# Performance work log

Measured on AMD Instinct MI355X. Metric: run time of the kernel, lower is better.

## Reference

```python
import jax, jax.numpy as jnp
import numpy as np

EPS = 1e-5

def conv1x1(x, W, b):
    # x: [B,C,H,W], W: [O,C], b: [O] -- a 1x1 conv is a per-pixel matmul
    return jnp.einsum('bchw,oc->bohw', x, W) + b[None, :, None, None]

def mean_variance_norm(feat):
    # torch .var(dim=2) is unbiased (ddof=1)
    m = feat.mean(axis=(2, 3), keepdims=True)
    v = feat.var(axis=(2, 3), ddof=1, keepdims=True)
    return (feat - m) / jnp.sqrt(v + EPS)

def setup_inputs() -> dict:
    key = jax.random.key(0)
    ks = jax.random.split(key, 10)
    B, C, H, W = 4, 256, 64, 64
    sc = 1.0 / np.sqrt(C)
    return {
        'content': jax.random.normal(ks[0], (B, C, H, W), jnp.float32),
        'style': jax.random.normal(ks[1], (B, C, H, W), jnp.float32),
        'content_key': jax.random.normal(ks[2], (B, C, H, W), jnp.float32),
        'style_key': jax.random.normal(ks[3], (B, C, H, W), jnp.float32),
        'Wf': jax.random.normal(ks[4], (C, C), jnp.float32) * sc,
        'bf': jnp.zeros((C,), jnp.float32),
        'Wg': jax.random.normal(ks[5], (C, C), jnp.float32) * sc,
        'bg': jnp.zeros((C,), jnp.float32),
        'Wh': jax.random.normal(ks[6], (C, C), jnp.float32) * sc,
        'bh': jnp.zeros((C,), jnp.float32),
    }

def reference(content, style, content_key, style_key, Wf, bf, Wg, bg, Wh, bh):
    Fq = conv1x1(content_key, Wf, bf)   # [B,Ck,H,W]
    G = conv1x1(style_key, Wg, bg)      # [B,Ck,Hs,Ws]
    Hv = conv1x1(style, Wh, bh)         # [B,C,Hs,Ws]
    b, _, h, w = Fq.shape
    _, C, hs, ws = Hv.shape
    N, M = h * w, hs * ws
    q = Fq.reshape(b, -1, N).transpose(0, 2, 1)   # [B,N,Ck]
    k = G.reshape(b, -1, M)                        # [B,Ck,M]
    style_flat = Hv.reshape(b, C, M).transpose(0, 2, 1)  # [B,M,C]
    # masks are all-ones -> attn_mask all zeros -> no masking (faithful to None path)
    S = jax.nn.softmax(jnp.einsum('bnc,bcm->bnm', q, k), axis=-1)  # [B,N,M]
    mean = jnp.einsum('bnm,bmc->bnc', S, style_flat)               # [B,N,C]
    std = jnp.sqrt(jax.nn.relu(
        jnp.einsum('bnm,bmc->bnc', S, style_flat * style_flat) - mean * mean))
    mean = mean.reshape(b, h, w, C).transpose(0, 3, 1, 2)  # [B,C,H,W]
    std = std.reshape(b, h, w, C).transpose(0, 3, 1, 2)
    return std * mean_variance_norm(content) + mean
```

## Files before the change

### kernel.cpp

```cpp
#include <hip/hip_runtime.h>


typedef unsigned int u32;
typedef unsigned short u16;
typedef _Float16 f16x8 __attribute__((ext_vector_type(8)));
typedef float f32x4 __attribute__((ext_vector_type(4)));
typedef float f32x16 __attribute__((ext_vector_type(16)));
typedef unsigned int u32x2 __attribute__((ext_vector_type(2)));
typedef unsigned __attribute__((address_space(3))) as3_u32;
typedef const unsigned __attribute__((address_space(1))) as1_u32;

#define L2E 1.44269504088896340736f
#define MFMA(a, b, c) __builtin_amdgcn_mfma_f32_16x16x32_f16(a, b, c, 0, 0, 0)
#define MFMA32(a, b, c) __builtin_amdgcn_mfma_f32_32x32x16_f16(a, b, c, 0, 0, 0)
#define EXP2(x) __builtin_amdgcn_exp2f(x)

__device__ __forceinline__ u16 h_bits(_Float16 h) { return __builtin_bit_cast(u16, h); }
__device__ __forceinline__ u16 f2h(float f) { return h_bits((_Float16)f); }
__device__ __forceinline__ u32 pk2(float a, float b) {
    return (u32)f2h(a) | ((u32)f2h(b) << 16);
}

__device__ __forceinline__ f16x8 ldh8(const u16* p) {
    uint4 v = *(const uint4*)p;
    return __builtin_bit_cast(f16x8, v);
}

__device__ __forceinline__ void gll16(const u16* g, const void* lds) {
    __builtin_amdgcn_global_load_lds((as1_u32*)g,
                                     (as3_u32*)(unsigned)(unsigned long long)lds,
                                     16, 0, 0);
}

__device__ __forceinline__ u32x2 pl32_swap(u32 a, u32 b) {
#if __has_builtin(__builtin_amdgcn_permlane32_swap)
    return __builtin_amdgcn_permlane32_swap(a, b, false, false);
#else
    asm("v_permlane32_swap_b32 %0, %1" : "+v"(a), "+v"(b));
    u32x2 r; r.x = a; r.y = b; return r;
#endif
}

__global__ void k_prep(const float* __restrict__ content,
                       const float* __restrict__ style, const float* __restrict__ ckey,
                       const float* __restrict__ skey,
                       const float* __restrict__ Wf, const float* __restrict__ Wg,
                       const float* __restrict__ Wh,
                       u16* __restrict__ X1, u16* __restrict__ X2, u16* __restrict__ Cc,
                       u16* __restrict__ Wb,
                       float* __restrict__ cm, float* __restrict__ cr) {
    int z = blockIdx.z, t = threadIdx.x;
    if (z >= 15) {
        int blk = (z - 15) * 256 + blockIdx.y * 64 + blockIdx.x;
        const float* p = content + (size_t)blk * 4096;
        float s = 0.f, ss = 0.f;
        for (int i = 0; i < 4; i++) {
            float4 v = *(const float4*)(p + (i * 256 + t) * 4);
            s  += (v.x + v.y) + (v.z + v.w);
            ss += (v.x * v.x + v.y * v.y) + (v.z * v.z + v.w * v.w);
        }
        for (int d = 32; d >= 1; d >>= 1) { s += __shfl_xor(s, d); ss += __shfl_xor(ss, d); }
        __shared__ __align__(16) float as[4], ass[4];
        int w = t >> 6;
        if ((t & 63) == 0) { as[w] = s; ass[w] = ss; }
        __syncthreads();
        if (t == 0) {
            s  = (as[0] + as[1]) + (as[2] + as[3]);
            ss = (ass[0] + ass[1]) + (ass[2] + ass[3]);
            float mean = s * (1.0f / 4096.0f);
            float var = (ss - s * mean) * (1.0f / 4095.0f);
            cm[blk] = mean;
            cr[blk] = rsqrtf(var + 1e-5f);
        }
        return;
    }
    if (z >= 12) {
        if (blockIdx.y != 0) return;
        int m = z - 12;
        const float* src = (m == 0) ? Wf : ((m == 1) ? Wg : Wh);
        u16* dst = Wb + m * 65536;
        int i = (blockIdx.x * 256 + t) * 4;
        float4 v = *(const float4*)(src + i);
        ushort4 o;
        o.x = f2h(v.x); o.y = f2h(v.y); o.z = f2h(v.z); o.w = f2h(v.w);
        *(ushort4*)(dst + i) = o;
        return;
    }
    int tensor = z >> 2, b = z & 3;
    const float* src = ((tensor == 0) ? style : ((tensor == 1) ? ckey : skey))
                       + (size_t)b * 256 * 4096;
    u16* dst = ((tensor == 0) ? X1 : ((tensor == 1) ? X2 : Cc)) + (size_t)b * 4096 * 256;
    int c0 = blockIdx.y * 64, t0 = blockIdx.x * 64;
    __shared__ __align__(16) float ls[64][65];
    int tr = t >> 4, tc = t & 15;
    for (int i = 0; i < 4; i++) {
        int c_off = i * 16 + tr;
        float4 v = *(const float4*)(src + (size_t)(c0 + c_off) * 4096 + t0 + tc * 4);
        ls[tc * 4 + 0][c_off] = v.x;
        ls[tc * 4 + 1][c_off] = v.y;
        ls[tc * 4 + 2][c_off] = v.z;
        ls[tc * 4 + 3][c_off] = v.w;
    }
    __syncthreads();
    for (int i = 0; i < 4; i++) {
        int tokrow = i * 16 + tr;
        ushort4 o;
        o.x = f2h(ls[tokrow][tc * 4 + 0]);
        o.y = f2h(ls[tokrow][tc * 4 + 1]);
        o.z = f2h(ls[tokrow][tc * 4 + 2]);
        o.w = f2h(ls[tokrow][tc * 4 + 3]);
        *(ushort4*)(dst + (size_t)(t0 + tokrow) * 256 + c0 + tc * 4) = o;
    }
}

__launch_bounds__(256)
__global__ void k_gemm(const u16* X1, const u16* X2, u16* Cc,
                       u16* A, u16* Bv, const u16* __restrict__ Wb,
                       const float* __restrict__ bfp, const float* __restrict__ bgp,
                       const float* __restrict__ bhp) {
    int mode = blockIdx.z, b = blockIdx.y, tok0 = blockIdx.x * 64;
    const u16* X = ((mode == 0) ? X2 : ((mode == 1) ? (const u16*)Cc : X1))
                   + (size_t)b * 4096 * 256;
    const u16* W = Wb + mode * 65536;
    const float* bias = (mode == 0) ? bfp : ((mode == 1) ? bgp : bhp);
    int t = threadIdx.x, w = t >> 6, lane = t & 63, ln = lane & 15, quad = lane >> 4;

    f32x4 acc[4][4];
    for (int i = 0; i < 4; i++)
        for (int j = 0; j < 4; j++) acc[i][j] = f32x4{0.f, 0.f, 0.f, 0.f};

    #pragma unroll
    for (int ks = 0; ks < 8; ks++) {
        f16x8 wf[4];
        #pragma unroll
        for (int ct = 0; ct < 4; ct++)
            wf[ct] = ldh8(W + (size_t)(w * 64 + ct * 16 + ln) * 256 + ks * 32 + quad * 8);
        #pragma unroll
        for (int rt = 0; rt < 4; rt++) {
            f16x8 xf = ldh8(X + (size_t)(tok0 + rt * 16 + ln) * 256 + ks * 32 + quad * 8);
            if (mode < 2) {
                #pragma unroll
                for (int ct = 0; ct < 4; ct++) acc[rt][ct] = MFMA(xf, wf[ct], acc[rt][ct]);
            } else {
                #pragma unroll
                for (int ct = 0; ct < 4; ct++) acc[rt][ct] = MFMA(wf[ct], xf, acc[rt][ct]);
            }
        }
    }

    __syncthreads();

    if (mode < 2) {
        u16* O = ((mode == 0) ? A : Cc) + (size_t)b * 4096 * 256;
        float bv[4];
        #pragma unroll
        for (int ct = 0; ct < 4; ct++) bv[ct] = bias[w * 64 + ct * 16 + ln];
        #pragma unroll
        for (int rt = 0; rt < 4; rt++)
            #pragma unroll
            for (int ct = 0; ct < 4; ct++)
                #pragma unroll
                for (int r = 0; r < 4; r++) {
                    int tok = tok0 + rt * 16 + quad * 4 + r;
                    int o = w * 64 + ct * 16 + ln;
                    O[(size_t)tok * 256 + o] = f2h(acc[rt][ct][r] + bv[ct]);
                }
    } else {
        u16* OV = Bv + (size_t)b * 256 * 4096;
        #pragma unroll
        for (int ct = 0; ct < 4; ct++)
            #pragma unroll
            for (int r = 0; r < 4; r++) {
                int o = w * 64 + ct * 16 + quad * 4 + r;
                float bb = bias[o];
                #pragma unroll
                for (int rt = 0; rt < 4; rt++) {
                    int tok = tok0 + rt * 16 + ln;
                    OV[(size_t)o * 4096 + tok] = f2h(acc[rt][ct][r] + bb);
                }
            }
    }
}

__launch_bounds__(512)
__attribute__((amdgpu_waves_per_eu(2)))
__global__ void k_flash(const u16* __restrict__ Qt, const u16* __restrict__ Kt,
                        const u16* __restrict__ Vt,
                        const float* __restrict__ content, const float* __restrict__ cm,
                        const float* __restrict__ cr, float* __restrict__ out) {
    __shared__ __align__(16) char smem[131072];
    const u16* KsU = (const u16*)smem;
    int t = threadIdx.x, w8 = t >> 6, l = t & 63, lq = l & 31, h = l >> 5;
    int qg = w8 & 3, mh = w8 >> 2;

    int b = blockIdx.y, q0 = blockIdx.x * 128, coff = blockIdx.z * 128;

    const u16* Kg = Kt + (size_t)b * 4096 * 256;
    const u16* Vg = Vt + ((size_t)b * 256 + coff) * 4096;

    const u16* ksrc;
    {
        int qb = w8 * 1024 + l * 16;
        int r0 = qb >> 9;
        int swz = (qb & 511) ^ ((r0 & 7) << 4);
        ksrc = Kg + r0 * 256 + (swz >> 1);
    }
    const char* ldsKw = smem + w8 * 1024;

    int uu = (h ^ (lq & 7)) << 3;
    int tab0 = uu, tab1 = 16 ^ uu, tab2 = 32 ^ uu, tab3 = 48 ^ uu;
    int kb0 = (mh * 64 + lq) * 256;

    f16x8 qf[16];
    {
        const u16* qp = Qt + ((size_t)b * 4096 + q0 + qg * 32 + lq) * 256 + h * 8;
        #pragma unroll
        for (int ks = 0; ks < 16; ks++) qf[ks] = ldh8(qp + ks * 16);
    }

    f32x16 am[4], aq[4];
    #pragma unroll
    for (int i = 0; i < 16; i++) {
        am[0][i] = 0.f; am[1][i] = 0.f; am[2][i] = 0.f; am[3][i] = 0.f;
        aq[0][i] = 0.f; aq[1][i] = 0.f; aq[2][i] = 0.f; aq[3][i] = 0.f;
    }
    float mrow = -1e30f, lrow = 0.f;

    #pragma unroll
    for (int i = 0; i < 8; i++) gll16(ksrc + i * 4096, ldsKw + i * 8192);
    asm volatile("s_waitcnt vmcnt(0)" ::: "memory");
    __builtin_amdgcn_s_barrier();

    int koffB = 0;
    for (int it = 0; it < 32; it++) {
        if (it < 31) {
            int m0n = (it + 1) * 32768;
            #pragma unroll
            for (int i = 0; i < 8; i++)
                gll16(ksrc + m0n + i * 4096, ldsKw + (koffB ^ 65536) + i * 8192);
        }
        asm volatile("" ::: "memory");

        #pragma unroll
        for (int ph = 0; ph < 2; ph++) {
            int kb = (koffB >> 1) + kb0 + ph * 8192;
            f32x16 sA, sB;
            #pragma unroll
            for (int i = 0; i < 16; i++) { sA[i] = 0.f; sB[i] = 0.f; }
            __builtin_amdgcn_s_setprio(1);
            #pragma unroll
            for (int ks = 0; ks < 8; ks++) {
                int off = ((ks & 3) == 0 ? tab0 : (ks & 3) == 1 ? tab1
                          : (ks & 3) == 2 ? tab2 : tab3) + (ks >> 2) * 64;
                sA = MFMA32(ldh8(KsU + kb + off), qf[ks], sA);
            }
            #pragma unroll
            for (int ks = 8; ks < 16; ks++) {
                int off = ((ks & 3) == 0 ? tab0 : (ks & 3) == 1 ? tab1
                          : (ks & 3) == 2 ? tab2 : tab3) + (ks >> 2) * 64;
                sB = MFMA32(ldh8(KsU + kb + off), qf[ks], sB);
            }
            __builtin_amdgcn_s_setprio(0);
            f32x16 s;
            #pragma unroll
            for (int i = 0; i < 16; i++) s[i] = sA[i] + sB[i];

            const u16* Vit = Vg + it * 128 + mh * 64 + ph * 32;
            f16x8 vfr[2][4];
            #pragma unroll
            for (int ks = 0; ks < 2; ks++)
                #pragma unroll
                for (int ct = 0; ct < 4; ct++)
                    vfr[ks][ct] = ldh8(Vit + (size_t)(ct * 32 + lq) * 4096 + ks * 16 + h * 8);

            float m8[8];
            #pragma unroll
            for (int r = 0; r < 8; r++) m8[r] = fmaxf(s[r], s[r + 8]);
            #pragma unroll
            for (int d = 4; d >= 1; d >>= 1)
                #pragma unroll
                for (int r = 0; r < d; r++) m8[r] = fmaxf(m8[r], m8[r + d]);
            float mt = fmaxf(m8[0], __shfl_xor(m8[0], 32));

            float mn, al;
            bool resc = !__all(mt - mrow <= 8.0f);
            if (resc) {
                mn = fmaxf(mrow, mt);
                al = EXP2((mrow - mn) * L2E);
                mrow = mn;
            } else {
                mn = mrow;
                al = 1.0f;
            }
            float base = mn * L2E;
            #pragma unroll
            for (int r = 0; r < 16; r++)
                s[r] = (float)(_Float16)EXP2(__builtin_fmaf(s[r], L2E, -base));
            float a8[8];
            #pragma unroll
            for (int r = 0; r < 8; r++) a8[r] = s[r] + s[r + 8];
            #pragma unroll
            for (int d = 4; d >= 1; d >>= 1)
                #pragma unroll
                for (int r = 0; r < d; r++) a8[r] += a8[r + d];
            float rs = a8[0] + __shfl_xor(a8[0], 32);
            lrow = lrow * al + rs;

            if (resc) {
                #pragma unroll
                for (int r = 0; r < 16; r++) {
                    float sc = __shfl(al, 8 * (r >> 2) + 4 * h + (r & 3));
                    am[0][r] *= sc; am[1][r] *= sc; am[2][r] *= sc; am[3][r] *= sc;
                    aq[0][r] *= sc; aq[1][r] *= sc; aq[2][r] *= sc; aq[3][r] *= sc;
                }
            }

            f16x8 pfr[2];
            {
                u32 d0 = pk2(s[0], s[1]),   d1 = pk2(s[2], s[3]);
                u32 d2 = pk2(s[4], s[5]),   d3 = pk2(s[6], s[7]);
                u32 d4 = pk2(s[8], s[9]),   d5 = pk2(s[10], s[11]);
                u32 d6 = pk2(s[12], s[13]), d7 = pk2(s[14], s[15]);
                u32x2 p02 = pl32_swap(d0, d2);
                u32x2 p13 = pl32_swap(d1, d3);
                u32x2 p46 = pl32_swap(d4, d6);
                u32x2 p57 = pl32_swap(d5, d7);
                uint4 fa = {p02.x, p13.x, p02.y, p13.y};
                uint4 fb = {p46.x, p57.x, p46.y, p57.y};
                pfr[0] = __builtin_bit_cast(f16x8, fa);
                pfr[1] = __builtin_bit_cast(f16x8, fb);
            }

            __builtin_amdgcn_s_setprio(1);
            #pragma unroll
            for (int ks = 0; ks < 2; ks++) {
                f16x8 pf = pfr[ks];
                #pragma unroll
                for (int ct = 0; ct < 4; ct++) {
                    f16x8 vf = vfr[ks][ct];
                    am[ct] = MFMA32(pf, vf, am[ct]);
                    f16x8 vh = vf * vf;
                    f16x8 vl = __builtin_elementwise_fma(vf, vf, -vh);
                    aq[ct] = MFMA32(pf, vh, aq[ct]);
                    aq[ct] = MFMA32(pf, vl, aq[ct]);
                }
            }
            __builtin_amdgcn_s_setprio(0);
        }

        asm volatile("s_waitcnt vmcnt(0)" ::: "memory");
        __builtin_amdgcn_s_barrier();
        koffB ^= 65536;
    }

    float* P1  = (float*)smem;
    float* Lsm = (float*)(smem + 32768);
    float* Ms  = (float*)(smem + 36864);
    float* Ss  = (float*)(smem + 70656);
    __syncthreads();
    if (h == 0) {
        Lsm[w8 * 32 + lq] = lrow;
        Lsm[256 + w8 * 32 + lq] = mrow;
    }
    __syncthreads();
    int pw = w8 ^ 4;
    float lP = Lsm[pw * 32 + lq];
    float mP = Lsm[256 + pw * 32 + lq];
    float M = fmaxf(mrow, mP);
    float scOwn = EXP2((mrow - M) * L2E);
    float lC = lrow * scOwn + lP * EXP2((mP - M) * L2E);
    {
        #pragma unroll
        for (int r = 0; r < 16; r++) {
            float sc = __shfl(scOwn, 8 * (r >> 2) + 4 * h + (r & 3));
            am[0][r] *= sc; am[1][r] *= sc; am[2][r] *= sc; am[3][r] *= sc;
            aq[0][r] *= sc; aq[1][r] *= sc; aq[2][r] *= sc; aq[3][r] *= sc;
        }
    }
    float inv = 1.0f / lC;
    float iv[16];
    #pragma unroll
    for (int r = 0; r < 16; r++) iv[r] = __shfl(inv, (r & 3) + 8 * (r >> 2) + 4 * h);

    #pragma unroll
    for (int g = 0; g < 2; g++) {
        #pragma unroll
        for (int ct = 0; ct < 2; ct++) {
            int a = 2 * g + ct;
            __syncthreads();
            if (mh == 1) {
                #pragma unroll
                for (int rq = 0; rq < 4; rq++) {
                    int o = qg * 1024 + lq * 32 + 8 * rq + 4 * h;
                    f32x4 va = {am[a][4 * rq], am[a][4 * rq + 1],
                                am[a][4 * rq + 2], am[a][4 * rq + 3]};
                    f32x4 vq = {aq[a][4 * rq], aq[a][4 * rq + 1],
                                aq[a][4 * rq + 2], aq[a][4 * rq + 3]};
                    *(f32x4*)(P1 + o) = va;
                    *(f32x4*)(P1 + 4096 + o) = vq;
                }
            }
            __syncthreads();
            if (mh == 0) {
                #pragma unroll
                for (int rq = 0; rq < 4; rq++) {
                    int o = qg * 1024 + lq * 32 + 8 * rq + 4 * h;
                    f32x4 va = *(const f32x4*)(P1 + o);
                    f32x4 vq = *(const f32x4*)(P1 + 4096 + o);
                    #pragma unroll
                    for (int j = 0; j < 4; j++) {
                        am[a][4 * rq + j] += va[j];
                        aq[a][4 * rq + j] += vq[j];
                    }
                }
            }
        }
        __syncthreads();
        if (mh == 0) {
            #pragma unroll
            for (int ct = 0; ct < 2; ct++) {
                int a = 2 * g + ct;
                #pragma unroll
                for (int rq = 0; rq < 4; rq++) {
                    f32x4 mv, sv;
                    #pragma unroll
                    for (int j = 0; j < 4; j++) {
                        int r = 4 * rq + j;
                        float mean = am[a][r] * iv[r];
                        float ex2 = aq[a][r] * iv[r];
                        float var = ex2 - mean * mean;
                        mv[j] = mean;
                        sv[j] = sqrtf(fmaxf(var, 0.f));
                    }
                    int c = ct * 32 + lq;
                    int qloc = qg * 32 + 8 * rq + 4 * h;
                    *(f32x4*)(Ms + c * 132 + qloc) = mv;
                    *(f32x4*)(Ss + c * 132 + qloc) = sv;
                }
            }
        }
        __syncthreads();
        #pragma unroll
        for (int pass = 0; pass < 4; pass++) {
            int c = pass * 16 + (t >> 5);
            int qloc = (t & 31) * 4;
            f32x4 mv = *(const f32x4*)(Ms + c * 132 + qloc);
            f32x4 sv = *(const f32x4*)(Ss + c * 132 + qloc);
            int gc = coff + g * 64 + c;
            size_t basei = ((size_t)b * 256 + gc) * 4096 + q0 + qloc;
            float4 cv = *(const float4*)(content + basei);
            float cmv = cm[b * 256 + gc], crv = cr[b * 256 + gc];
            float4 o;
            o.x = sv[0] * ((cv.x - cmv) * crv) + mv[0];
            o.y = sv[1] * ((cv.y - cmv) * crv) + mv[1];
            o.z = sv[2] * ((cv.z - cmv) * crv) + mv[2];
            o.w = sv[3] * ((cv.w - cmv) * crv) + mv[3];
            *(float4*)(out + basei) = o;
        }
    }
}

extern "C" void kernel_launch(void* const* d_in, const int* in_sizes, int n_in,
                              void* d_out, int out_size, void* d_ws, size_t ws_size,
                              hipStream_t stream) {
    const float* content = (const float*)d_in[0];
    const float* style   = (const float*)d_in[1];
    const float* ckey    = (const float*)d_in[2];
    const float* skey    = (const float*)d_in[3];
    const float* Wf      = (const float*)d_in[4];
    const float* bfp     = (const float*)d_in[5];
    const float* Wg      = (const float*)d_in[6];
    const float* bgp     = (const float*)d_in[7];
    const float* Wh      = (const float*)d_in[8];
    const float* bhp     = (const float*)d_in[9];
    float* out = (float*)d_out;
    char* ws = (char*)d_ws;

    float* cm = (float*)(ws + 0);
    float* cr = (float*)(ws + 4096);
    u16*   Wb = (u16*)(ws + 8192);
    u16*   A  = (u16*)(ws + 1048576);
    u16*   Bv = (u16*)(ws + 9437184);
    u16*   Cc = (u16*)(ws + 17825792);
    u16*   X1 = (u16*)d_out;
    u16*   X2 = (u16*)d_out + 4194304;

    k_prep<<<dim3(64, 4, 19), 256, 0, stream>>>(content, style, ckey, skey,
                                                Wf, Wg, Wh, X1, X2, Cc, Wb, cm, cr);
    k_gemm<<<dim3(64, 4, 3), 256, 0, stream>>>(X1, X2, Cc, A, Bv, Wb, bfp, bgp, bhp);
    k_flash<<<dim3(32, 4, 2), 512, 0, stream>>>(A, Cc, Bv, content, cm, cr, out);
}
```

Baseline: 405.6 us.

## Stage V tiles through LDS with async global-to-LDS loads and swizzle

V fragments were previously read straight from global memory into registers inside the inner loop. Now each iteration loads the 128-column V tile into a new 32 KB swizzled LDS region using async global-to-LDS loads, issued before the K prefetch, and the PV MFMAs read from LDS after a waitcnt and barrier. The aim is coalesced V loads and less global-load latency exposed in the inner loop. In exchange, LDS use grows to 160 KB per block and an extra barrier is added per iteration. The K prefetch now also runs on the last iteration, wrapping to tile 0, which adds redundant loads.

Measured after the change: 339.3 us. 1.2x faster.

```diff
diff --git a/kernel.cpp b/kernel.cpp
--- a/kernel.cpp
+++ b/kernel.cpp
@@ -188,7 +188,7 @@
                         const u16* __restrict__ Vt,
                         const float* __restrict__ content, const float* __restrict__ cm,
                         const float* __restrict__ cr, float* __restrict__ out) {
-    __shared__ __align__(16) char smem[131072];
+    __shared__ __align__(16) char smem[163840];
     const u16* KsU = (const u16*)smem;
     int t = threadIdx.x, w8 = t >> 6, l = t & 63, lq = l & 31, h = l >> 5;
     int qg = w8 & 3, mh = w8 >> 2;
@@ -207,6 +207,20 @@
     }
     const char* ldsKw = smem + w8 * 1024;
 
+    const char* ldsVw = smem + 131072 + w8 * 4096;
+    int vrow0 = w8 * 16 + (l >> 4);
+    int vs0, vs1, vs2, vs3;
+    {
+        int r0v = vrow0,     k0v = ((l & 15) ^ (r0v & 15)) << 3;
+        int r1v = vrow0 + 4, k1v = ((l & 15) ^ (r1v & 15)) << 3;
+        int r2v = vrow0 + 8, k2v = ((l & 15) ^ (r2v & 15)) << 3;
+        int r3v = vrow0 + 12, k3v = ((l & 15) ^ (r3v & 15)) << 3;
+        vs0 = r0v * 4096 + k0v; vs1 = r1v * 4096 + k1v;
+        vs2 = r2v * 4096 + k2v; vs3 = r3v * 4096 + k3v;
+    }
+    int vb16 = 65536 + lq * 128;
+    int vcb  = ((mh << 3) | h) ^ (lq & 15);
+
     int uu = (h ^ (lq & 7)) << 3;
     int tab0 = uu, tab1 = 16 ^ uu, tab2 = 32 ^ uu, tab3 = 48 ^ uu;
     int kb0 = (mh * 64 + lq) * 256;
@@ -233,8 +247,16 @@
 
     int koffB = 0;
     for (int it = 0; it < 32; it++) {
-        if (it < 31) {
-            int m0n = (it + 1) * 32768;
+        {
+            int m0v = it * 128;
+            gll16(Vg + vs0 + m0v, ldsVw + 0);
+            gll16(Vg + vs1 + m0v, ldsVw + 1024);
+            gll16(Vg + vs2 + m0v, ldsVw + 2048);
+            gll16(Vg + vs3 + m0v, ldsVw + 3072);
+        }
+        asm volatile("" ::: "memory");
+        {
+            int m0n = ((it + 1) & 31) * 32768;
             #pragma unroll
             for (int i = 0; i < 8; i++)
                 gll16(ksrc + m0n + i * 4096, ldsKw + (koffB ^ 65536) + i * 8192);
@@ -264,14 +286,6 @@
             f32x16 s;
             #pragma unroll
             for (int i = 0; i < 16; i++) s[i] = sA[i] + sB[i];
-
-            const u16* Vit = Vg + it * 128 + mh * 64 + ph * 32;
-            f16x8 vfr[2][4];
-            #pragma unroll
-            for (int ks = 0; ks < 2; ks++)
-                #pragma unroll
-                for (int ct = 0; ct < 4; ct++)
-                    vfr[ks][ct] = ldh8(Vit + (size_t)(ct * 32 + lq) * 4096 + ks * 16 + h * 8);
 
             float m8[8];
             #pragma unroll
@@ -331,13 +345,22 @@
                 pfr[1] = __builtin_bit_cast(f16x8, fb);
             }
 
+            if (ph == 0) {
+                asm volatile("s_waitcnt vmcnt(8)" ::: "memory");
+                __builtin_amdgcn_s_barrier();
+                asm volatile("" ::: "memory");
+            }
+
             __builtin_amdgcn_s_setprio(1);
             #pragma unroll
             for (int ks = 0; ks < 2; ks++) {
                 f16x8 pf = pfr[ks];
+                int col = (vcb ^ (ph << 2) ^ (ks << 1)) << 3;
                 #pragma unroll
                 for (int ct = 0; ct < 4; ct++) {
-                    f16x8 vf = vfr[ks][ct];
+                    f16x8 vf = ldh8(KsU + vb16 + ct * 4096 +
+                                    (((vcb ^ (ph << 2) ^ (ks << 1))) << 3));
+                    (void)col;
                     am[ct] = MFMA32(pf, vf, am[ct]);
                     f16x8 vh = vf * vf;
                     f16x8 vl = __builtin_elementwise_fma(vf, vf, -vh);
```
